# Kernel tuning notes

Measured on AMD Instinct MI355X. Metric: run time of the kernel, lower is better.

Reference implementation:

```python
import jax, jax.numpy as jnp
import numpy as np

EMBED_DIM = 768
VOCAB = 4096
HID = 128
B, N = 8, 4096


def setup_inputs() -> dict:
    key = jax.random.key(0)
    ks = jax.random.split(key, 12)
    s = lambda k, sh, fan_in: jax.random.normal(k, sh, jnp.float32) * (1.0 / np.sqrt(fan_in))
    return {
        "coordinates": jax.random.normal(ks[0], (B, N, 2), jnp.float32),
        "features": jax.random.normal(ks[1], (B, N, 10), jnp.float32),
        # spatial encoder: Linear(2,128) -> ReLU -> Linear(128,768); weights stored [in,out]
        "Ws1": s(ks[2], (2, HID), 2), "bs1": jnp.zeros((HID,), jnp.float32),
        "Ws2": s(ks[3], (HID, EMBED_DIM), HID), "bs2": jnp.zeros((EMBED_DIM,), jnp.float32),
        # feature encoder: Linear(10,128) -> ReLU -> Linear(128,768)
        "Wf1": s(ks[4], (10, HID), 10), "bf1": jnp.zeros((HID,), jnp.float32),
        "Wf2": s(ks[5], (HID, EMBED_DIM), HID), "bf2": jnp.zeros((EMBED_DIM,), jnp.float32),
        # quantizer codebook (nn.Embedding weight)
        "codebook": jax.random.normal(ks[6], (VOCAB, EMBED_DIM), jnp.float32),
    }


def reference(coordinates, features, Ws1, bs1, Ws2, bs2, Wf1, bf1, Wf2, bf2, codebook):
    spatial_emb = jax.nn.relu(coordinates @ Ws1 + bs1) @ Ws2 + bs2   # [B,N,D]
    feature_emb = jax.nn.relu(features @ Wf1 + bf1) @ Wf2 + bf2     # [B,N,D]
    combined = spatial_emb + feature_emb                             # [B,N,D]
    # squared euclidean distances (argmin is invariant to sqrt / -||x||^2 term)
    x_sq = jnp.sum(combined * combined, axis=-1, keepdims=True)      # [B,N,1]
    c_sq = jnp.sum(codebook * codebook, axis=-1)                     # [V]
    dots = jnp.einsum('bnd,vd->bnv', combined, codebook)             # [B,N,V]
    dists = x_sq - 2.0 * dots + c_sq                                 # [B,N,V]
    tokens = jnp.argmin(dists, axis=-1)                              # [B,N] int
    quantized = codebook[tokens]                                     # [B,N,D]
    return tokens, quantized
```

## Files before the change

kernel.cpp:

```cpp
#include <hip/hip_runtime.h>
#include <hip/hip_bf16.h>
#include <cfloat>

#define M_ROWS 32768
#define DIM    768
#define VOCABN 4096
#define HIDN   128
#define QB     64
#define CAP    32
#define MARGIN 2.0f

#define BM 128
#define BN 128
#define NCB (VOCABN / BN)
#define CAP2 6
#define NKC  (DIM / 32)

typedef __attribute__((ext_vector_type(8))) short bf16x8;
typedef __attribute__((ext_vector_type(4))) float f32x4;

static __device__ __forceinline__ short f2b(float x) {
    __hip_bfloat16 h = __float2bfloat16(x);
    return *reinterpret_cast<short*>(&h);
}


__global__ __launch_bounds__(256) void encode_kernel(
    const float* __restrict__ coords, const float* __restrict__ feats,
    const float* __restrict__ Ws1, const float* __restrict__ bs1,
    const float* __restrict__ Ws2, const float* __restrict__ bs2,
    const float* __restrict__ Wf1, const float* __restrict__ bf1,
    const float* __restrict__ Wf2, const float* __restrict__ bf2,
    float* __restrict__ comb, short* __restrict__ comb16f, int write16)
{
    __shared__ float hs[32][HIDN];
    __shared__ float hf[32][HIDN];
    const int row0 = blockIdx.x * 32;
    const int t = threadIdx.x;

    #pragma unroll
    for (int k = 0; k < 16; ++k) {
        const int idx = t + k * 256;
        const int r = idx >> 7;
        const int j = idx & 127;
        const int row = row0 + r;
        const float c0 = coords[row * 2 + 0];
        const float c1 = coords[row * 2 + 1];
        float vs = fmaf(c0, Ws1[j], fmaf(c1, Ws1[HIDN + j], bs1[j]));
        hs[r][j] = fmaxf(vs, 0.0f);
        float vf = bf1[j];
        #pragma unroll
        for (int i = 0; i < 10; ++i)
            vf = fmaf(feats[row * 10 + i], Wf1[i * HIDN + j], vf);
        hf[r][j] = fmaxf(vf, 0.0f);
    }
    __syncthreads();

    float acc[3][32];
    #pragma unroll
    for (int dd = 0; dd < 3; ++dd) {
        const float base = bs2[t + dd * 256] + bf2[t + dd * 256];
        #pragma unroll
        for (int r = 0; r < 32; ++r) acc[dd][r] = base;
    }

    for (int jq = 0; jq < 32; ++jq) {
        float ws[3][4], wf[3][4];
        #pragma unroll
        for (int dd = 0; dd < 3; ++dd) {
            const int d = t + dd * 256;
            #pragma unroll
            for (int jj = 0; jj < 4; ++jj) {
                ws[dd][jj] = Ws2[(jq * 4 + jj) * DIM + d];
                wf[dd][jj] = Wf2[(jq * 4 + jj) * DIM + d];
            }
        }
        #pragma unroll
        for (int r = 0; r < 32; ++r) {
            const float4 h4s = *(const float4*)&hs[r][jq * 4];
            const float4 h4f = *(const float4*)&hf[r][jq * 4];
            #pragma unroll
            for (int dd = 0; dd < 3; ++dd) {
                float a = acc[dd][r];
                a = fmaf(h4s.x, ws[dd][0], a);
                a = fmaf(h4s.y, ws[dd][1], a);
                a = fmaf(h4s.z, ws[dd][2], a);
                a = fmaf(h4s.w, ws[dd][3], a);
                a = fmaf(h4f.x, wf[dd][0], a);
                a = fmaf(h4f.y, wf[dd][1], a);
                a = fmaf(h4f.z, wf[dd][2], a);
                a = fmaf(h4f.w, wf[dd][3], a);
                acc[dd][r] = a;
            }
        }
    }

    const int qt = row0 >> 7;
    #pragma unroll
    for (int dd = 0; dd < 3; ++dd) {
        const int d = t + dd * 256;
        const int kc = d >> 5, kg = (d >> 3) & 3, jj = d & 7;
        #pragma unroll
        for (int r = 0; r < 32; ++r) {
            const int row = row0 + r;
            const float v = acc[dd][r];
            comb[(size_t)row * DIM + d] = v;
            if (write16) {
                const int it = (row >> 4) & 7, n = row & 15;
                const size_t unit = ((size_t)(qt * 8 + it) * NKC + kc) * 64 + kg * 16 + n;
                comb16f[unit * 8 + jj] = f2b(v);
            }
        }
    }
}

__global__ __launch_bounds__(64) void csq_cvt_kernel(
    const float* __restrict__ codebook, float* __restrict__ csq,
    short* __restrict__ outb, int swizzled)
{
    const int v = blockIdx.x;
    const int l = threadIdx.x;
    float s = 0.0f;
    #pragma unroll
    for (int k = 0; k < DIM / 64; ++k) {
        const float x = codebook[(size_t)v * DIM + l + k * 64];
        if (!swizzled) outb[(size_t)v * DIM + l + k * 64] = f2b(x);
        s = fmaf(x, x, s);
    }
    #pragma unroll
    for (int off = 32; off >= 1; off >>= 1)
        s += __shfl_down(s, off);
    if (l == 0) csq[v] = s;

    if (swizzled) {
        const int cb = v >> 7, jt = (v >> 4) & 7, n = v & 15;
        for (int u = l; u < 96; u += 64) {
            const int kc = u >> 2, kg = u & 3;
            const float* src = codebook + (size_t)v * DIM + kc * 32 + kg * 8;
            bf16x8 f;
            #pragma unroll
            for (int j = 0; j < 8; ++j) f[j] = f2b(src[j]);
            const size_t unit = ((size_t)(cb * 8 + jt) * NKC + kc) * 64 + kg * 16 + n;
            *(bf16x8*)(outb + unit * 8) = f;
        }
    }
}

__global__ __launch_bounds__(256) void vq_phase1_kernel(
    const short* __restrict__ comb16f, const short* __restrict__ cbf,
    const float* __restrict__ csq,
    float* __restrict__ lmin_g, int* __restrict__ lbidx_g,
    int* __restrict__ lcnt_g, int* __restrict__ lci_g)
{
    __shared__ float s_wmin[2][BM];
    __shared__ int   s_widx[2][BM];
    __shared__ float s_thr[BM];
    __shared__ int   s_cnt[BM];
    __shared__ int   s_ci[BM][CAP2];

    const int t = threadIdx.x;
    const int w = t >> 6, l = t & 63;
    const int lm = l & 15, quad = l >> 4;
    const int wr = w & 1, wc = w >> 1;
    const int cb = blockIdx.x;
    const int qt = blockIdx.y;
    const int q0 = qt * BM;

    if (t < BM) s_cnt[t] = 0;

    const short* ap[4];
    const short* bp[4];
    #pragma unroll
    for (int i = 0; i < 4; ++i) {
        ap[i] = comb16f + (((size_t)(qt * 8 + wr * 4 + i) * NKC) * 64 + l) * 8;
        bp[i] = cbf     + (((size_t)(cb * 8 + wc * 4 + i) * NKC) * 64 + l) * 8;
    }

    f32x4 acc[4][4];
    #pragma unroll
    for (int i = 0; i < 4; ++i)
        #pragma unroll
        for (int j = 0; j < 4; ++j) acc[i][j] = (f32x4){0.f, 0.f, 0.f, 0.f};

    #pragma unroll 2
    for (int kc = 0; kc < NKC; ++kc) {
        bf16x8 a[4], b[4];
        #pragma unroll
        for (int i = 0; i < 4; ++i) a[i] = *(const bf16x8*)(ap[i] + kc * 512);
        #pragma unroll
        for (int j = 0; j < 4; ++j) b[j] = *(const bf16x8*)(bp[j] + kc * 512);
        #pragma unroll
        for (int i = 0; i < 4; ++i)
            #pragma unroll
            for (int j = 0; j < 4; ++j)
                acc[i][j] = __builtin_amdgcn_mfma_f32_16x16x32_bf16(
                    a[i], b[j], acc[i][j], 0, 0, 0);
    }

    const int cbase = cb * BN + wc * 64;
    float cs[4];
    #pragma unroll
    for (int j = 0; j < 4; ++j) cs[j] = csq[cbase + j * 16 + lm];
    #pragma unroll
    for (int i = 0; i < 4; ++i)
        #pragma unroll
        for (int j = 0; j < 4; ++j)
            #pragma unroll
            for (int r = 0; r < 4; ++r)
                acc[i][j][r] = fmaf(-2.0f, acc[i][j][r], cs[j]);

    #pragma unroll
    for (int i = 0; i < 4; ++i)
        #pragma unroll
        for (int r = 0; r < 4; ++r) {
            float m = acc[i][0][r];
            int mi = cbase + 0 * 16 + lm;
            #pragma unroll
            for (int j = 1; j < 4; ++j) {
                const float d = acc[i][j][r];
                const int ci = cbase + j * 16 + lm;
                if (d < m || (d == m && ci < mi)) { m = d; mi = ci; }
            }
            #pragma unroll
            for (int off = 1; off <= 8; off <<= 1) {
                const float om = __shfl_xor(m, off);
                const int oi = __shfl_xor(mi, off);
                if (om < m || (om == m && oi < mi)) { m = om; mi = oi; }
            }
            if (lm == 0) {
                const int qloc = wr * 64 + i * 16 + quad * 4 + r;
                s_wmin[wc][qloc] = m;
                s_widx[wc][qloc] = mi;
            }
        }
    __syncthreads();

    if (t < BM) {
        const float v0 = s_wmin[0][t], v1 = s_wmin[1][t];
        const int i0 = s_widx[0][t], i1 = s_widx[1][t];
        const float bm = fminf(v0, v1);
        const int bi = (v1 < v0 || (v1 == v0 && i1 < i0)) ? i1 : i0;
        const size_t base = (size_t)cb * M_ROWS + (q0 + t);
        lmin_g[base] = bm;
        lbidx_g[base] = bi;
        s_thr[t] = bm + MARGIN;
    }
    __syncthreads();

    #pragma unroll
    for (int i = 0; i < 4; ++i)
        #pragma unroll
        for (int r = 0; r < 4; ++r) {
            const int qloc = wr * 64 + i * 16 + quad * 4 + r;
            const float thr = s_thr[qloc];
            #pragma unroll
            for (int j = 0; j < 4; ++j) {
                const float d = acc[i][j][r];
                if (d <= thr) {
                    const int p = atomicAdd(&s_cnt[qloc], 1);
                    if (p < CAP2) s_ci[qloc][p] = cbase + j * 16 + lm;
                }
            }
        }
    __syncthreads();

    if (t < BM) {
        const size_t base = (size_t)cb * M_ROWS + (q0 + t);
        int n = s_cnt[t];
        if (n > CAP2) n = CAP2;
        lcnt_g[base] = n;
        for (int p = 0; p < n; ++p)
            lci_g[base * CAP2 + p] = s_ci[t][p];
    }
}

#define P2CAP 48
__global__ __launch_bounds__(256) void vq_phase2_kernel(
    const float* __restrict__ comb32, const float* __restrict__ codebook,
    const float* __restrict__ csq,
    const float* __restrict__ lmin_g, const int* __restrict__ lbidx_g,
    const int* __restrict__ lcnt_g, const int* __restrict__ lci_g,
    float* __restrict__ out_tok_f, float* __restrict__ out_q)
{
    __shared__ int s2n[4];
    __shared__ int s2c[4][P2CAP];
    const int t = threadIdx.x, w = t >> 6, l = t & 63;
    const int q = blockIdx.x * 4 + w;
    if (l == 0) s2n[w] = 0;

    const size_t base = (size_t)l * M_ROWS + q;
    const float v = (l < NCB) ? lmin_g[base] : FLT_MAX;
    float g = v;
    #pragma unroll
    for (int off = 1; off <= 32; off <<= 1)
        g = fminf(g, __shfl_xor(g, off));
    const float thr = g + MARGIN;

    if (l < NCB && v <= thr) {
        int p = atomicAdd(&s2n[w], 1);
        if (p < P2CAP) s2c[w][p] = lbidx_g[base];
        int n = lcnt_g[base];
        if (n > CAP2) n = CAP2;
        for (int e = 0; e < n; ++e) {
            p = atomicAdd(&s2n[w], 1);
            if (p < P2CAP) s2c[w][p] = lci_g[base * CAP2 + e];
        }
    }
    __syncthreads();

    int ns = s2n[w];
    if (ns > P2CAP) ns = P2CAP;
    float bestd = FLT_MAX;
    int bestc = 0x7fffffff;
    const float4* xr = (const float4*)(comb32 + (size_t)q * DIM);
    for (int e = 0; e < ns; ++e) {
        const int c = s2c[w][e];
        const float4* cr = (const float4*)(codebook + (size_t)c * DIM);
        float dot = 0.0f;
        #pragma unroll
        for (int k = 0; k < 3; ++k) {
            const float4 x = xr[l + 64 * k];
            const float4 y = cr[l + 64 * k];
            dot = fmaf(x.x, y.x, fmaf(x.y, y.y, fmaf(x.z, y.z, fmaf(x.w, y.w, dot))));
        }
        #pragma unroll
        for (int off = 1; off <= 32; off <<= 1)
            dot += __shfl_xor(dot, off);
        const float d = fmaf(-2.0f, dot, csq[c]);
        if (d < bestd || (d == bestd && c < bestc)) { bestd = d; bestc = c; }
    }
    if (l == 0) out_tok_f[q] = (float)bestc;
    const float4* cr = (const float4*)(codebook + (size_t)bestc * DIM);
    float4* o4 = (float4*)(out_q + (size_t)q * DIM);
    #pragma unroll
    for (int k = 0; k < 3; ++k) o4[l + 64 * k] = cr[l + 64 * k];
}

__global__ __launch_bounds__(256) void argmin_mfma_kernel(
    const float* __restrict__ comb, const float* __restrict__ codebook,
    const short* __restrict__ cbb, const float* __restrict__ csq,
    float* __restrict__ out_tok_f, int* __restrict__ tok_i)
{
    __shared__ int s_cnt[QB];
    __shared__ int s_cand[QB][CAP];

    const int t = threadIdx.x;
    const int w = t >> 6;
    const int l = t & 63;
    const int lm = l & 15;
    const int quad = l >> 4;
    const int q0 = blockIdx.x * QB;

    for (int i = t; i < QB; i += 256) s_cnt[i] = 0;
    __syncthreads();

    bf16x8 a_reg[24];
    {
        const int qa = q0 + w * 16 + lm;
        const float* ap = comb + (size_t)qa * DIM + quad * 8;
        #pragma unroll
        for (int kc = 0; kc < 24; ++kc) {
            const float4 lo = *(const float4*)(ap + kc * 32);
            const float4 hi = *(const float4*)(ap + kc * 32 + 4);
            bf16x8 f;
            f[0] = f2b(lo.x); f[1] = f2b(lo.y); f[2] = f2b(lo.z); f[3] = f2b(lo.w);
            f[4] = f2b(hi.x); f[5] = f2b(hi.y); f[6] = f2b(hi.z); f[7] = f2b(hi.w);
            a_reg[kc] = f;
        }
    }

    const short* bp = cbb + (size_t)lm * DIM + quad * 8;
    float runmin[4] = {FLT_MAX, FLT_MAX, FLT_MAX, FLT_MAX};

    for (int chunk = 0; chunk < VOCABN / 64; ++chunk) {
        const int c0 = chunk * 64;
        const short* bc = bp + (size_t)c0 * DIM;
        f32x4 acc[4];
        #pragma unroll
        for (int s = 0; s < 4; ++s) acc[s] = (f32x4){0.f, 0.f, 0.f, 0.f};

        #pragma unroll
        for (int kc = 0; kc < 24; ++kc) {
            const bf16x8 a = a_reg[kc];
            #pragma unroll
            for (int s = 0; s < 4; ++s) {
                const bf16x8 b = *(const bf16x8*)(bc + s * 16 * DIM + kc * 32);
                acc[s] = __builtin_amdgcn_mfma_f32_16x16x32_bf16(a, b, acc[s], 0, 0, 0);
            }
        }

        float d[4][4];
        float m[4] = {FLT_MAX, FLT_MAX, FLT_MAX, FLT_MAX};
        #pragma unroll
        for (int s = 0; s < 4; ++s) {
            const float csv = csq[c0 + s * 16 + lm];
            #pragma unroll
            for (int r = 0; r < 4; ++r) {
                d[s][r] = fmaf(-2.0f, acc[s][r], csv);
                m[r] = fminf(m[r], d[s][r]);
            }
        }
        #pragma unroll
        for (int r = 0; r < 4; ++r) {
            float vv = m[r];
            vv = fminf(vv, __shfl_xor(vv, 1));
            vv = fminf(vv, __shfl_xor(vv, 2));
            vv = fminf(vv, __shfl_xor(vv, 4));
            vv = fminf(vv, __shfl_xor(vv, 8));
            runmin[r] = fminf(runmin[r], vv);
        }
        #pragma unroll
        for (int s = 0; s < 4; ++s) {
            #pragma unroll
            for (int r = 0; r < 4; ++r) {
                if (d[s][r] <= runmin[r] + MARGIN) {
                    const int qloc = w * 16 + quad * 4 + r;
                    const int idx = atomicAdd(&s_cnt[qloc], 1);
                    if (idx < CAP) s_cand[qloc][idx] = c0 + s * 16 + lm;
                }
            }
        }
    }
    __syncthreads();

    const int qloc = t >> 2;
    const int sub = t & 3;
    const int qg = q0 + qloc;
    int n = s_cnt[qloc];
    if (n > CAP) n = CAP;
    float bestd = FLT_MAX;
    int bestc = 0x7fffffff;
    const float4* xr = (const float4*)(comb + (size_t)qg * DIM);
    for (int i = 0; i < n; ++i) {
        const int c = s_cand[qloc][i];
        const float4* cr = (const float4*)(codebook + (size_t)c * DIM);
        float dot = 0.0f;
        #pragma unroll 4
        for (int j = sub * 48; j < sub * 48 + 48; ++j) {
            const float4 x = xr[j];
            const float4 y = cr[j];
            dot = fmaf(x.x, y.x, fmaf(x.y, y.y, fmaf(x.z, y.z, fmaf(x.w, y.w, dot))));
        }
        dot += __shfl_xor(dot, 1);
        dot += __shfl_xor(dot, 2);
        const float dist = fmaf(-2.0f, dot, csq[c]);
        if (dist < bestd || (dist == bestd && c < bestc)) { bestd = dist; bestc = c; }
    }
    if (sub == 0) {
        out_tok_f[qg] = (float)bestc;
        tok_i[qg] = bestc;
    }
}

__global__ __launch_bounds__(192) void gather_kernel(
    const int* __restrict__ tok, const float* __restrict__ codebook,
    float* __restrict__ outq)
{
    const int row = blockIdx.x;
    const int t = threadIdx.x;
    const int token = tok[row];
    const float4* cb4 = (const float4*)(codebook + (size_t)token * DIM);
    float4* o4 = (float4*)(outq + (size_t)row * DIM);
    o4[t] = cb4[t];
}

extern "C" void kernel_launch(void* const* d_in, const int* in_sizes, int n_in,
                              void* d_out, int out_size, void* d_ws, size_t ws_size,
                              hipStream_t stream) {
    const float* coords   = (const float*)d_in[0];
    const float* feats    = (const float*)d_in[1];
    const float* Ws1      = (const float*)d_in[2];
    const float* bs1      = (const float*)d_in[3];
    const float* Ws2      = (const float*)d_in[4];
    const float* bs2      = (const float*)d_in[5];
    const float* Wf1      = (const float*)d_in[6];
    const float* bf1      = (const float*)d_in[7];
    const float* Wf2      = (const float*)d_in[8];
    const float* bf2      = (const float*)d_in[9];
    const float* codebook = (const float*)d_in[10];

    float* out = (float*)d_out;
    float* out_tok = out;
    float* out_q   = out + M_ROWS;

    const size_t SZ_COMB32 = (size_t)M_ROWS * DIM * 4;
    const size_t SZ_COMB16 = (size_t)M_ROWS * DIM * 2;
    const size_t SZ_CBB    = (size_t)VOCABN * DIM * 2;
    const size_t SZ_CSQ    = (size_t)VOCABN * 4;
    const size_t SZ_LMIN   = (size_t)M_ROWS * NCB * 4;
    const size_t SZ_LCI    = (size_t)M_ROWS * NCB * CAP2 * 4;
    const size_t NEED = SZ_COMB32 + SZ_COMB16 + SZ_CBB + SZ_CSQ +
                        3 * SZ_LMIN + SZ_LCI;

    char* p = (char*)d_ws;
    float* comb32 = (float*)p;              p += SZ_COMB32;
    short* comb16f = (short*)p;             p += SZ_COMB16;
    short* cbx = (short*)p;                 p += SZ_CBB;
    float* csq = (float*)p;                 p += SZ_CSQ;

    if (ws_size >= NEED) {
        float* lmin_g = (float*)p;          p += SZ_LMIN;
        int*   lbidx_g = (int*)p;           p += SZ_LMIN;
        int*   lcnt_g = (int*)p;            p += SZ_LMIN;
        int*   lci_g = (int*)p;             p += SZ_LCI;

        encode_kernel<<<M_ROWS / 32, 256, 0, stream>>>(
            coords, feats, Ws1, bs1, Ws2, bs2, Wf1, bf1, Wf2, bf2,
            comb32, comb16f, 1);
        csq_cvt_kernel<<<VOCABN, 64, 0, stream>>>(codebook, csq, cbx, 1);
        dim3 g1(NCB, M_ROWS / BM, 1);
        vq_phase1_kernel<<<g1, 256, 0, stream>>>(
            comb16f, cbx, csq, lmin_g, lbidx_g, lcnt_g, lci_g);
        vq_phase2_kernel<<<M_ROWS / 4, 256, 0, stream>>>(
            comb32, codebook, csq, lmin_g, lbidx_g, lcnt_g, lci_g,
            out_tok, out_q);
    } else {
        int* toki = (int*)p;
        encode_kernel<<<M_ROWS / 32, 256, 0, stream>>>(
            coords, feats, Ws1, bs1, Ws2, bs2, Wf1, bf1, Wf2, bf2,
            comb32, comb16f, 0);
        csq_cvt_kernel<<<VOCABN, 64, 0, stream>>>(codebook, csq, cbx, 0);
        argmin_mfma_kernel<<<M_ROWS / QB, 256, 0, stream>>>(
            comb32, codebook, cbx, csq, out_tok, toki);
        gather_kernel<<<M_ROWS, 192, 0, stream>>>(toki, codebook, out_q);
    }
}
```

Before: 706.0 us.

## Stage phase-1 GEMM tiles through LDS with async global-to-LDS 4-deep pipeline

The phase-1 distance GEMM now uses 256x256 tiles with 512 threads per block. Operand fragments are loaded with direct global-to-LDS transfers into a four-buffer ring, three stages ahead, using explicit vmcnt waits and barriers. Before, each wave loaded its operands straight from global memory. The larger tile halves the number of codebook chunks and so shrinks the per-chunk candidate arrays that phase 2 reads. The cost is 128KB of LDS per block, more accumulator registers, and a hand-counted waitcnt schedule that is fragile.

```diff
diff --git a/kernel.cpp b/kernel.cpp
--- a/kernel.cpp
+++ b/kernel.cpp
@@ -10,9 +10,9 @@
 #define CAP    32
 #define MARGIN 2.0f
 
-#define BM 128
-#define BN 128
-#define NCB (VOCABN / BN)
+#define BM2 256
+#define BN2 256
+#define NCB2 (VOCABN / BN2)
 #define CAP2 6
 #define NKC  (DIM / 32)
 
@@ -22,6 +22,12 @@
 static __device__ __forceinline__ short f2b(float x) {
     __hip_bfloat16 h = __float2bfloat16(x);
     return *reinterpret_cast<short*>(&h);
+}
+
+static __device__ __forceinline__ void gload_lds16(const void* g, void* l) {
+    __builtin_amdgcn_global_load_lds(
+        (const __attribute__((address_space(1))) unsigned int*)g,
+        (__attribute__((address_space(3))) unsigned int*)l, 16, 0, 0);
 }
 
 
@@ -146,63 +152,100 @@
     }
 }
 
-__global__ __launch_bounds__(256) void vq_phase1_kernel(
+__global__ __launch_bounds__(512, 2) void vq_phase1_kernel(
     const short* __restrict__ comb16f, const short* __restrict__ cbf,
     const float* __restrict__ csq,
     float* __restrict__ lmin_g, int* __restrict__ lbidx_g,
     int* __restrict__ lcnt_g, int* __restrict__ lci_g)
 {
-    __shared__ float s_wmin[2][BM];
-    __shared__ int   s_widx[2][BM];
-    __shared__ float s_thr[BM];
-    __shared__ int   s_cnt[BM];
-    __shared__ int   s_ci[BM][CAP2];
+    __shared__ __align__(16) char smem[4 * 32768];
 
     const int t = threadIdx.x;
     const int w = t >> 6, l = t & 63;
     const int lm = l & 15, quad = l >> 4;
-    const int wr = w & 1, wc = w >> 1;
+    const int wr = w >> 2, wc = w & 3;
     const int cb = blockIdx.x;
     const int qt = blockIdx.y;
-    const int q0 = qt * BM;
-
-    if (t < BM) s_cnt[t] = 0;
-
-    const short* ap[4];
-    const short* bp[4];
-    #pragma unroll
-    for (int i = 0; i < 4; ++i) {
-        ap[i] = comb16f + (((size_t)(qt * 8 + wr * 4 + i) * NKC) * 64 + l) * 8;
-        bp[i] = cbf     + (((size_t)(cb * 8 + wc * 4 + i) * NKC) * 64 + l) * 8;
-    }
-
-    f32x4 acc[4][4];
-    #pragma unroll
-    for (int i = 0; i < 4; ++i)
+    const int q0 = qt * BM2;
+
+    const short* gsrc[4];
+    int doff[4];
+    #pragma unroll
+    for (int k = 0; k < 4; ++k) {
+        const int s = w * 4 + k;
+        if (s < 16) {
+            gsrc[k] = comb16f + (((size_t)(qt * 16 + s) * NKC) * 64 + l) * 8;
+            doff[k] = s * 1024;
+        } else {
+            gsrc[k] = cbf + (((size_t)(cb * 16 + (s - 16)) * NKC) * 64 + l) * 8;
+            doff[k] = 16384 + (s - 16) * 1024;
+        }
+    }
+
+    f32x4 acc[8][4];
+    #pragma unroll
+    for (int i = 0; i < 8; ++i)
         #pragma unroll
         for (int j = 0; j < 4; ++j) acc[i][j] = (f32x4){0.f, 0.f, 0.f, 0.f};
 
-    #pragma unroll 2
+    #define STAGE(kc) do {                                                      \
+        char* _d = smem + ((kc) & 3) * 32768;                                   \
+        _Pragma("unroll")                                                       \
+        for (int _k = 0; _k < 4; ++_k)                                          \
+            gload_lds16(gsrc[_k] + (size_t)(kc) * 512, _d + doff[_k]);          \
+    } while (0)
+
+    STAGE(0); STAGE(1); STAGE(2);
+    asm volatile("s_waitcnt vmcnt(8)" ::: "memory");
+    __builtin_amdgcn_sched_barrier(0);
+    __builtin_amdgcn_s_barrier();
+    __builtin_amdgcn_sched_barrier(0);
+
+    #pragma unroll
     for (int kc = 0; kc < NKC; ++kc) {
-        bf16x8 a[4], b[4];
-        #pragma unroll
-        for (int i = 0; i < 4; ++i) a[i] = *(const bf16x8*)(ap[i] + kc * 512);
-        #pragma unroll
-        for (int j = 0; j < 4; ++j) b[j] = *(const bf16x8*)(bp[j] + kc * 512);
-        #pragma unroll
-        for (int i = 0; i < 4; ++i)
+        if (kc + 3 < NKC) STAGE(kc + 3);
+        const char* buf = smem + (kc & 3) * 32768;
+        bf16x8 a[8], b[4];
+        #pragma unroll
+        for (int i = 0; i < 8; ++i)
+            a[i] = *(const bf16x8*)(buf + (wr * 8 + i) * 1024 + l * 16);
+        #pragma unroll
+        for (int j = 0; j < 4; ++j)
+            b[j] = *(const bf16x8*)(buf + 16384 + (wc * 4 + j) * 1024 + l * 16);
+        __builtin_amdgcn_s_setprio(1);
+        #pragma unroll
+        for (int i = 0; i < 8; ++i)
             #pragma unroll
             for (int j = 0; j < 4; ++j)
                 acc[i][j] = __builtin_amdgcn_mfma_f32_16x16x32_bf16(
                     a[i], b[j], acc[i][j], 0, 0, 0);
-    }
-
-    const int cbase = cb * BN + wc * 64;
+        __builtin_amdgcn_s_setprio(0);
+        if (kc < NKC - 1) {
+            if (kc <= NKC - 4)      asm volatile("s_waitcnt vmcnt(8)" ::: "memory");
+            else if (kc == NKC - 3) asm volatile("s_waitcnt vmcnt(4)" ::: "memory");
+            else                    asm volatile("s_waitcnt vmcnt(0)" ::: "memory");
+            __builtin_amdgcn_sched_barrier(0);
+            __builtin_amdgcn_s_barrier();
+            __builtin_amdgcn_sched_barrier(0);
+        }
+    }
+    #undef STAGE
+
+    float* s_wmin = (float*)smem;
+    int*   s_widx = (int*)(smem + 4096);
+    float* s_thr  = (float*)(smem + 8192);
+    int*   s_cnt  = (int*)(smem + 9216);
+    int*   s_ci   = (int*)(smem + 10240);
+
+    __syncthreads();
+    if (t < BM2) s_cnt[t] = 0;
+
+    const int cbase = cb * BN2 + wc * 64;
     float cs[4];
     #pragma unroll
     for (int j = 0; j < 4; ++j) cs[j] = csq[cbase + j * 16 + lm];
     #pragma unroll
-    for (int i = 0; i < 4; ++i)
+    for (int i = 0; i < 8; ++i)
         #pragma unroll
         for (int j = 0; j < 4; ++j)
             #pragma unroll
@@ -210,7 +253,7 @@
                 acc[i][j][r] = fmaf(-2.0f, acc[i][j][r], cs[j]);
 
     #pragma unroll
-    for (int i = 0; i < 4; ++i)
+    for (int i = 0; i < 8; ++i)
         #pragma unroll
         for (int r = 0; r < 4; ++r) {
             float m = acc[i][0][r];
@@ -228,18 +271,22 @@
                 if (om < m || (om == m && oi < mi)) { m = om; mi = oi; }
             }
             if (lm == 0) {
-                const int qloc = wr * 64 + i * 16 + quad * 4 + r;
-                s_wmin[wc][qloc] = m;
-                s_widx[wc][qloc] = mi;
-            }
-        }
-    __syncthreads();
-
-    if (t < BM) {
-        const float v0 = s_wmin[0][t], v1 = s_wmin[1][t];
-        const int i0 = s_widx[0][t], i1 = s_widx[1][t];
-        const float bm = fminf(v0, v1);
-        const int bi = (v1 < v0 || (v1 == v0 && i1 < i0)) ? i1 : i0;
+                const int qloc = wr * 128 + i * 16 + quad * 4 + r;
+                s_wmin[wc * 256 + qloc] = m;
+                s_widx[wc * 256 + qloc] = mi;
+            }
+        }
+    __syncthreads();
+
+    if (t < BM2) {
+        float bm = s_wmin[t];
+        int bi = s_widx[t];
+        #pragma unroll
+        for (int g2 = 1; g2 < 4; ++g2) {
+            const float v = s_wmin[g2 * 256 + t];
+            const int ii = s_widx[g2 * 256 + t];
+            if (v < bm || (v == bm && ii < bi)) { bm = v; bi = ii; }
+        }
         const size_t base = (size_t)cb * M_ROWS + (q0 + t);
         lmin_g[base] = bm;
         lbidx_g[base] = bi;
@@ -248,29 +295,29 @@
     __syncthreads();
 
     #pragma unroll
-    for (int i = 0; i < 4; ++i)
+    for (int i = 0; i < 8; ++i)
         #pragma unroll
         for (int r = 0; r < 4; ++r) {
-            const int qloc = wr * 64 + i * 16 + quad * 4 + r;
+            const int qloc = wr * 128 + i * 16 + quad * 4 + r;
             const float thr = s_thr[qloc];
             #pragma unroll
             for (int j = 0; j < 4; ++j) {
                 const float d = acc[i][j][r];
                 if (d <= thr) {
                     const int p = atomicAdd(&s_cnt[qloc], 1);
-                    if (p < CAP2) s_ci[qloc][p] = cbase + j * 16 + lm;
+                    if (p < CAP2) s_ci[qloc * CAP2 + p] = cbase + j * 16 + lm;
                 }
             }
         }
     __syncthreads();
 
-    if (t < BM) {
+    if (t < BM2) {
         const size_t base = (size_t)cb * M_ROWS + (q0 + t);
         int n = s_cnt[t];
         if (n > CAP2) n = CAP2;
         lcnt_g[base] = n;
         for (int p = 0; p < n; ++p)
-            lci_g[base * CAP2 + p] = s_ci[t][p];
+            lci_g[base * CAP2 + p] = s_ci[t * CAP2 + p];
     }
 }
 
@@ -289,14 +336,14 @@
     if (l == 0) s2n[w] = 0;
 
     const size_t base = (size_t)l * M_ROWS + q;
-    const float v = (l < NCB) ? lmin_g[base] : FLT_MAX;
+    const float v = (l < NCB2) ? lmin_g[base] : FLT_MAX;
     float g = v;
     #pragma unroll
     for (int off = 1; off <= 32; off <<= 1)
         g = fminf(g, __shfl_xor(g, off));
     const float thr = g + MARGIN;
 
-    if (l < NCB && v <= thr) {
+    if (l < NCB2 && v <= thr) {
         int p = atomicAdd(&s2n[w], 1);
         if (p < P2CAP) s2c[w][p] = lbidx_g[base];
         int n = lcnt_g[base];
@@ -487,8 +534,8 @@
     const size_t SZ_COMB16 = (size_t)M_ROWS * DIM * 2;
     const size_t SZ_CBB    = (size_t)VOCABN * DIM * 2;
     const size_t SZ_CSQ    = (size_t)VOCABN * 4;
-    const size_t SZ_LMIN   = (size_t)M_ROWS * NCB * 4;
-    const size_t SZ_LCI    = (size_t)M_ROWS * NCB * CAP2 * 4;
+    const size_t SZ_LMIN   = (size_t)M_ROWS * NCB2 * 4;
+    const size_t SZ_LCI    = (size_t)M_ROWS * NCB2 * CAP2 * 4;
     const size_t NEED = SZ_COMB32 + SZ_COMB16 + SZ_CBB + SZ_CSQ +
                         3 * SZ_LMIN + SZ_LCI;
 
@@ -508,8 +555,8 @@
             coords, feats, Ws1, bs1, Ws2, bs2, Wf1, bf1, Wf2, bf2,
             comb32, comb16f, 1);
         csq_cvt_kernel<<<VOCABN, 64, 0, stream>>>(codebook, csq, cbx, 1);
-        dim3 g1(NCB, M_ROWS / BM, 1);
-        vq_phase1_kernel<<<g1, 256, 0, stream>>>(
+        dim3 g1(NCB2, M_ROWS / BM2, 1);
+        vq_phase1_kernel<<<g1, 512, 0, stream>>>(
             comb16f, cbx, csq, lmin_g, lbidx_g, lcnt_g, lci_g);
         vq_phase2_kernel<<<M_ROWS / 4, 256, 0, stream>>>(
             comb32, codebook, csq, lmin_g, lbidx_g, lcnt_g, lci_g,
```

New measurement: 678.4 us. 3.9% less time.

## Stage phase1 GEMM tiles through double-buffered LDS with direct global-to-LDS loads

Applied to the files above, without the earlier changes.

Phase1 now loads each block's A and B fragments for a k-chunk cooperatively into a double-buffered LDS area using global_load_lds, and every wave reads its operands from LDS. Before, each wave read its own fragments from global memory, so the same codebook and query tiles were fetched twice per block. The block index is also remapped to group query and codebook tiles for L2 locality, and launch bounds are raised to three blocks per SM. In exchange there is a barrier per k-chunk, 32KB of LDS per block, and tighter register limits that could cause spills.

```diff
diff --git a/kernel.cpp b/kernel.cpp
--- a/kernel.cpp
+++ b/kernel.cpp
@@ -10,9 +10,9 @@
 #define CAP    32
 #define MARGIN 2.0f
 
-#define BM 128
-#define BN 128
-#define NCB (VOCABN / BN)
+#define BM1 128
+#define BN1 128
+#define NCB (VOCABN / BN1)
 #define CAP2 6
 #define NKC  (DIM / 32)
 
@@ -22,6 +22,12 @@
 static __device__ __forceinline__ short f2b(float x) {
     __hip_bfloat16 h = __float2bfloat16(x);
     return *reinterpret_cast<short*>(&h);
+}
+
+static __device__ __forceinline__ void gload_lds16(const void* g, void* l) {
+    __builtin_amdgcn_global_load_lds(
+        (const __attribute__((address_space(1))) unsigned int*)g,
+        (__attribute__((address_space(3))) unsigned int*)l, 16, 0, 0);
 }
 
 
@@ -146,34 +152,39 @@
     }
 }
 
-__global__ __launch_bounds__(256) void vq_phase1_kernel(
+__global__ __launch_bounds__(256, 3) void vq_phase1_kernel(
     const short* __restrict__ comb16f, const short* __restrict__ cbf,
     const float* __restrict__ csq,
     float* __restrict__ lmin_g, int* __restrict__ lbidx_g,
     int* __restrict__ lcnt_g, int* __restrict__ lci_g)
 {
-    __shared__ float s_wmin[2][BM];
-    __shared__ int   s_widx[2][BM];
-    __shared__ float s_thr[BM];
-    __shared__ int   s_cnt[BM];
-    __shared__ int   s_ci[BM][CAP2];
+    __shared__ __align__(16) char smem[2 * 16384];
 
     const int t = threadIdx.x;
     const int w = t >> 6, l = t & 63;
     const int lm = l & 15, quad = l >> 4;
-    const int wr = w & 1, wc = w >> 1;
-    const int cb = blockIdx.x;
-    const int qt = blockIdx.y;
-    const int q0 = qt * BM;
-
-    if (t < BM) s_cnt[t] = 0;
-
-    const short* ap[4];
-    const short* bp[4];
-    #pragma unroll
-    for (int i = 0; i < 4; ++i) {
-        ap[i] = comb16f + (((size_t)(qt * 8 + wr * 4 + i) * NKC) * 64 + l) * 8;
-        bp[i] = cbf     + (((size_t)(cb * 8 + wc * 4 + i) * NKC) * 64 + l) * 8;
+    const int wr = w >> 1, wc = w & 1;
+
+    const int lin = blockIdx.y * (int)gridDim.x + blockIdx.x;
+    const int x  = lin & 7;
+    const int s_ = (lin >> 3) & 63;
+    const int r_ = lin >> 9;
+    const int qt = (r_ * 4 + (x >> 1)) * 4 + (s_ >> 4);
+    const int cb = (x & 1) * 16 + (s_ & 15);
+    const int q0 = qt * BM1;
+
+    const short* gsrc[4];
+    int doff[4];
+    #pragma unroll
+    for (int k = 0; k < 4; ++k) {
+        const int s = w * 4 + k;
+        if (s < 8) {
+            gsrc[k] = comb16f + (((size_t)(qt * 8 + s) * NKC) * 64 + l) * 8;
+            doff[k] = s * 1024;
+        } else {
+            gsrc[k] = cbf + (((size_t)(cb * 8 + (s - 8)) * NKC) * 64 + l) * 8;
+            doff[k] = 8192 + (s - 8) * 1024;
+        }
     }
 
     f32x4 acc[4][4];
@@ -182,22 +193,47 @@
         #pragma unroll
         for (int j = 0; j < 4; ++j) acc[i][j] = (f32x4){0.f, 0.f, 0.f, 0.f};
 
-    #pragma unroll 2
+    #define STAGE(kc) do {                                                      \
+        char* _d = smem + ((kc) & 1) * 16384;                                   \
+        _Pragma("unroll")                                                       \
+        for (int _k = 0; _k < 4; ++_k)                                          \
+            gload_lds16(gsrc[_k] + (size_t)(kc) * 512, _d + doff[_k]);          \
+    } while (0)
+
+    STAGE(0);
+    __syncthreads();
+
+    #pragma unroll
     for (int kc = 0; kc < NKC; ++kc) {
+        if (kc + 1 < NKC) STAGE(kc + 1);
+        const char* buf = smem + (kc & 1) * 16384;
         bf16x8 a[4], b[4];
         #pragma unroll
-        for (int i = 0; i < 4; ++i) a[i] = *(const bf16x8*)(ap[i] + kc * 512);
-        #pragma unroll
-        for (int j = 0; j < 4; ++j) b[j] = *(const bf16x8*)(bp[j] + kc * 512);
+        for (int i = 0; i < 4; ++i)
+            a[i] = *(const bf16x8*)(buf + (wr * 4 + i) * 1024 + l * 16);
+        #pragma unroll
+        for (int j = 0; j < 4; ++j)
+            b[j] = *(const bf16x8*)(buf + 8192 + (wc * 4 + j) * 1024 + l * 16);
         #pragma unroll
         for (int i = 0; i < 4; ++i)
             #pragma unroll
             for (int j = 0; j < 4; ++j)
                 acc[i][j] = __builtin_amdgcn_mfma_f32_16x16x32_bf16(
                     a[i], b[j], acc[i][j], 0, 0, 0);
-    }
-
-    const int cbase = cb * BN + wc * 64;
+        if (kc + 1 < NKC) __syncthreads();
+    }
+    #undef STAGE
+
+    float* s_wmin = (float*)smem;
+    int*   s_widx = (int*)(smem + 1024);
+    float* s_thr  = (float*)(smem + 2048);
+    int*   s_cnt  = (int*)(smem + 2560);
+    int*   s_ci   = (int*)(smem + 3072);
+
+    __syncthreads();
+    if (t < BM1) s_cnt[t] = 0;
+
+    const int cbase = cb * BN1 + wc * 64;
     float cs[4];
     #pragma unroll
     for (int j = 0; j < 4; ++j) cs[j] = csq[cbase + j * 16 + lm];
@@ -229,15 +265,15 @@
             }
             if (lm == 0) {
                 const int qloc = wr * 64 + i * 16 + quad * 4 + r;
-                s_wmin[wc][qloc] = m;
-                s_widx[wc][qloc] = mi;
-            }
-        }
-    __syncthreads();
-
-    if (t < BM) {
-        const float v0 = s_wmin[0][t], v1 = s_wmin[1][t];
-        const int i0 = s_widx[0][t], i1 = s_widx[1][t];
+                s_wmin[wc * 128 + qloc] = m;
+                s_widx[wc * 128 + qloc] = mi;
+            }
+        }
+    __syncthreads();
+
+    if (t < BM1) {
+        const float v0 = s_wmin[t], v1 = s_wmin[128 + t];
+        const int i0 = s_widx[t], i1 = s_widx[128 + t];
         const float bm = fminf(v0, v1);
         const int bi = (v1 < v0 || (v1 == v0 && i1 < i0)) ? i1 : i0;
         const size_t base = (size_t)cb * M_ROWS + (q0 + t);
@@ -258,19 +294,19 @@
                 const float d = acc[i][j][r];
                 if (d <= thr) {
                     const int p = atomicAdd(&s_cnt[qloc], 1);
-                    if (p < CAP2) s_ci[qloc][p] = cbase + j * 16 + lm;
+                    if (p < CAP2) s_ci[qloc * CAP2 + p] = cbase + j * 16 + lm;
                 }
             }
         }
     __syncthreads();
 
-    if (t < BM) {
+    if (t < BM1) {
         const size_t base = (size_t)cb * M_ROWS + (q0 + t);
         int n = s_cnt[t];
         if (n > CAP2) n = CAP2;
         lcnt_g[base] = n;
         for (int p = 0; p < n; ++p)
-            lci_g[base * CAP2 + p] = s_ci[t][p];
+            lci_g[base * CAP2 + p] = s_ci[t * CAP2 + p];
     }
 }
 
@@ -508,7 +544,7 @@
             coords, feats, Ws1, bs1, Ws2, bs2, Wf1, bf1, Wf2, bf2,
             comb32, comb16f, 1);
         csq_cvt_kernel<<<VOCABN, 64, 0, stream>>>(codebook, csq, cbx, 1);
-        dim3 g1(NCB, M_ROWS / BM, 1);
+        dim3 g1(NCB, M_ROWS / BM1, 1);
         vq_phase1_kernel<<<g1, 256, 0, stream>>>(
             comb16f, cbx, csq, lmin_g, lbidx_g, lcnt_g, lci_g);
         vq_phase2_kernel<<<M_ROWS / 4, 256, 0, stream>>>(
```

After: 665.5 us. 5.7% less time.
